# Performance work log

Hardware: AMD Instinct MI355X
Metric: run time of the kernel (lower is better)

Reference implementation:

```python
import jax, jax.numpy as jnp
import numpy as np

IN_DIM = 300   # args.glove_init == 1
MID_DIM = 450  # ceil(1.5 * 300)
BATCH = 131072
NEG_SLOPE = 0.1


def setup_inputs() -> dict:
    key = jax.random.key(0)
    ks = jax.random.split(key, 13)

    def W(k, o, i):
        return jax.random.normal(k, (o, i), jnp.float32) * (1.0 / np.sqrt(i).astype(np.float32))

    def b(k, o):
        return jax.random.normal(k, (o,), jnp.float32) * 0.01

    inp = {"x": jax.random.normal(ks[0], (BATCH, IN_DIM), jnp.float32)}
    # NOT_op: Linear(300->450), LeakyReLU(0.1), Linear(450->300), LeakyReLU(0.1)
    inp["not_W1"] = W(ks[1], MID_DIM, IN_DIM);      inp["not_b1"] = b(ks[2], MID_DIM)
    inp["not_W2"] = W(ks[3], IN_DIM, MID_DIM);      inp["not_b2"] = b(ks[4], IN_DIM)
    # AND_op: Linear(600->450), LeakyReLU, Linear(450->300), LeakyReLU
    inp["and_W1"] = W(ks[5], MID_DIM, 2 * IN_DIM);  inp["and_b1"] = b(ks[6], MID_DIM)
    inp["and_W2"] = W(ks[7], IN_DIM, MID_DIM);      inp["and_b2"] = b(ks[8], IN_DIM)
    # OR_op: same shapes as AND_op
    inp["or_W1"] = W(ks[9], MID_DIM, 2 * IN_DIM);   inp["or_b1"] = b(ks[10], MID_DIM)
    inp["or_W2"] = W(ks[11], IN_DIM, MID_DIM);      inp["or_b2"] = b(ks[12], IN_DIM)
    inp["epoch"] = 1  # epoch <= el_epochs -> el_forward path
    return inp


def _mlp(x, W1, b1, W2, b2):
    # torch Linear: y = x @ W.T + b; LeakyReLU(0.1)
    h = jax.nn.leaky_relu(x @ W1.T + b1, NEG_SLOPE)
    return jax.nn.leaky_relu(h @ W2.T + b2, NEG_SLOPE)


def reference(x, not_W1, not_b1, not_W2, not_b2,
              and_W1, and_b1, and_W2, and_b2,
              or_W1, or_b1, or_W2, or_b2, epoch):
    # el_forward, fully batched (original loops over samples):
    # pairs: (x, NOT(NOT(x))), (x, AND([x,x])), (x, OR([x,x])); MSE over all pairs.
    s2a = _mlp(_mlp(x, not_W1, not_b1, not_W2, not_b2), not_W1, not_b1, not_W2, not_b2)
    xx = jnp.concatenate([x, x], axis=-1)  # [B, 600]
    s2b = _mlp(xx, and_W1, and_b1, and_W2, and_b2)
    s2c = _mlp(xx, or_W1, or_b1, or_W2, or_b2)
    # mean over the stacked 3B pairs == mean of the three per-pair MSEs
    loss = (jnp.mean((x - s2a) ** 2)
            + jnp.mean((x - s2b) ** 2)
            + jnp.mean((x - s2c) ** 2)) / 3.0
    return loss
```

## Files before the change

### kernel.cpp

```cpp
#include <hip/hip_runtime.h>

typedef __attribute__((ext_vector_type(8))) short short8;
typedef __attribute__((ext_vector_type(4))) float f32x4;

#define BATCH   131072
#define IND     300
#define MIDD    450
#define XS      328
#define HS      488
#define BM      64
#define NTHR    512

constexpr int SZ1 = 464 * XS;
constexpr int SZ2 = 304 * HS;
constexpr int O_NOT1 = 0;
constexpr int O_NOT2 = SZ1;
constexpr int O_AND1 = SZ1 + SZ2;
constexpr int O_AND2 = 2 * SZ1 + SZ2;
constexpr int O_OR1  = 2 * SZ1 + 2 * SZ2;
constexpr int O_OR2  = 3 * SZ1 + 2 * SZ2;
constexpr int WS_ELEMS = 3 * SZ1 + 3 * SZ2;

constexpr int XBYTES = BM * XS * 2;
constexpr int HBYTES = BM * HS * 2;
constexpr int LDS_BYTES = XBYTES + HBYTES;

__device__ __forceinline__ unsigned short f2b(float f) {
  unsigned u = __builtin_bit_cast(unsigned, f);
  u = (u + 0x7FFFu + ((u >> 16) & 1u)) >> 16;
  return (unsigned short)u;
}
__device__ __forceinline__ float b2f(unsigned short h) {
  unsigned u = ((unsigned)h) << 16;
  return __builtin_bit_cast(float, u);
}
__device__ __forceinline__ f32x4 mfma16(short8 a, short8 b, f32x4 c) {
  asm("v_mfma_f32_16x16x32_bf16 %0, %1, %2, %0" : "+v"(c) : "v"(a), "v"(b));
  return c;
}

__global__ void prep_weights(const float* __restrict__ nw1, const float* __restrict__ nw2,
                             const float* __restrict__ aw1, const float* __restrict__ aw2,
                             const float* __restrict__ ow1, const float* __restrict__ ow2,
                             unsigned short* __restrict__ ws)
{
  int idx = blockIdx.x * 256 + threadIdx.x;
  if (idx < 3 * SZ1) {
    int r = idx / SZ1, off = idx % SZ1;
    int n = off / XS, k = off % XS;
    float v = 0.f;
    if (n < MIDD && k < IND) {
      if (r == 0) v = nw1[n * IND + k];
      else {
        const float* s = (r == 1) ? aw1 : ow1;
        v = s[n * 2 * IND + k] + s[n * 2 * IND + IND + k];
      }
    }
    int base = (r == 0) ? O_NOT1 : (r == 1) ? O_AND1 : O_OR1;
    ws[base + off] = f2b(v);
  } else if (idx < WS_ELEMS) {
    int i2 = idx - 3 * SZ1;
    int r = i2 / SZ2, off = i2 % SZ2;
    int n = off / HS, k = off % HS;
    float v = 0.f;
    if (n < IND && k < MIDD) {
      const float* s = (r == 0) ? nw2 : (r == 1) ? aw2 : ow2;
      v = s[n * MIDD + k];
    }
    int base = (r == 0) ? O_NOT2 : (r == 1) ? O_AND2 : O_OR2;
    ws[base + off] = f2b(v);
  }
}

template <int KB, int NT, int N, bool MSE>
__device__ __forceinline__ void stage(const unsigned short* __restrict__ IN, int in_stride,
                                      const unsigned short* __restrict__ Wg, int wg_stride,
                                      const float* __restrict__ bias,
                                      unsigned short* __restrict__ Hout,
                                      const unsigned short* __restrict__ XT,
                                      float& sq, int tid, int wn, int l16, int lhi)
{
  constexpr int NJ = (NT + 7) / 8;
  f32x4 acc[4][NJ];
#pragma unroll
  for (int m = 0; m < 4; m++)
#pragma unroll
    for (int j = 0; j < NJ; j++) acc[m][j] = f32x4{0.f, 0.f, 0.f, 0.f};

  const unsigned short* ap[4];
#pragma unroll
  for (int m = 0; m < 4; m++) ap[m] = IN + (m * 16 + l16) * in_stride + lhi * 8;
  const unsigned short* bp[NJ];
#pragma unroll
  for (int j = 0; j < NJ; j++) {
    int nt = wn + 8 * j;
    int row = (nt < NT ? nt : 0) * 16 + l16;
    bp[j] = Wg + row * wg_stride + lhi * 8;
  }

  short8 a0[4], a1[4], b0[NJ], b1[NJ], b2[NJ];

#define LA_(buf, kk)                                                     \
  { _Pragma("unroll") for (int m = 0; m < 4; m++)                        \
      buf[m] = *(const short8*)(ap[m] + (kk) * 32); }
#define LB_(buf, kk)                                                     \
  { _Pragma("unroll") for (int j = 0; j < NJ; j++)                       \
      if (wn + 8 * j < NT) buf[j] = *(const short8*)(bp[j] + (kk) * 32); }

  LB_(b0, 0);
  if (KB > 1) LB_(b1, 1);
  LA_(a0, 0);

#pragma unroll
  for (int kb = 0; kb < KB; kb++) {
    short8* ac = (kb & 1) ? a1 : a0;
    short8* an = (kb & 1) ? a0 : a1;
    short8* bc = (kb % 3 == 0) ? b0 : (kb % 3 == 1) ? b1 : b2;
    short8* bn = ((kb + 2) % 3 == 0) ? b0 : ((kb + 2) % 3 == 1) ? b1 : b2;
    if (kb + 2 < KB) LB_(bn, kb + 2);
    if (kb + 1 < KB) LA_(an, kb + 1);
#pragma unroll
    for (int j = 0; j < NJ; j++) {
      if (wn + 8 * j < NT) {
#pragma unroll
        for (int m = 0; m < 4; m++) acc[m][j] = mfma16(ac[m], bc[j], acc[m][j]);
      }
    }
  }
#undef LA_
#undef LB_

  if (!MSE) __syncthreads();

#pragma unroll
  for (int j = 0; j < NJ; j++) {
    int nt = wn + 8 * j;
    if (nt >= NT) continue;
    int col = nt * 16 + l16;
    bool valid = col < N;
    float bv = valid ? bias[col] : 0.f;
#pragma unroll
    for (int m = 0; m < 4; m++) {
#pragma unroll
      for (int r = 0; r < 4; r++) {
        int row = m * 16 + lhi * 4 + r;
        float v = acc[m][j][r] + bv;
        v = v > 0.f ? v : 0.1f * v;
        if (MSE) {
          if (valid) { float d = b2f(XT[row * XS + col]) - v; sq += d * d; }
        } else {
          if (valid) Hout[row * HS + col] = f2b(v);
        }
      }
    }
  }
  if (!MSE && N == IND) {
    for (int i = tid; i < BM * 20; i += NTHR) {
      int r = i / 20, c = i - r * 20;
      Hout[r * HS + IND + c] = 0;
    }
  }
}

__global__ __launch_bounds__(NTHR, 2)
void fused(const float* __restrict__ x, const unsigned short* __restrict__ ws,
           const float* __restrict__ nb1, const float* __restrict__ nb2,
           const float* __restrict__ ab1, const float* __restrict__ ab2,
           const float* __restrict__ ob1, const float* __restrict__ ob2,
           float* __restrict__ out)
{
  extern __shared__ __align__(16) char smem[];
  unsigned short* X = (unsigned short*)smem;
  unsigned short* H = (unsigned short*)(smem + XBYTES);
  int tid = threadIdx.x, wid = tid >> 6, lane = tid & 63;
  int l16 = lane & 15, lhi = lane >> 4;

  for (int i = tid; i < LDS_BYTES / 4; i += NTHR) ((unsigned*)smem)[i] = 0u;
  __syncthreads();

  int row0 = blockIdx.x * BM;
  for (int i = tid; i < BM * IND; i += NTHR) {
    int r = i / IND, c = i - r * IND;
    X[r * XS + c] = f2b(x[(row0 + r) * IND + c]);
  }
  __syncthreads();

  float sq = 0.f;
  stage<10, 29, MIDD, false>(X, XS, ws + O_NOT1, XS, nb1, H, X, sq, tid, wid, l16, lhi);
  __syncthreads();
  stage<15, 19, IND,  false>(H, HS, ws + O_NOT2, HS, nb2, H, X, sq, tid, wid, l16, lhi);
  __syncthreads();
  stage<10, 29, MIDD, false>(H, HS, ws + O_NOT1, XS, nb1, H, X, sq, tid, wid, l16, lhi);
  __syncthreads();
  stage<15, 19, IND,  true >(H, HS, ws + O_NOT2, HS, nb2, H, X, sq, tid, wid, l16, lhi);
  __syncthreads();
  stage<10, 29, MIDD, false>(X, XS, ws + O_AND1, XS, ab1, H, X, sq, tid, wid, l16, lhi);
  __syncthreads();
  stage<15, 19, IND,  true >(H, HS, ws + O_AND2, HS, ab2, H, X, sq, tid, wid, l16, lhi);
  __syncthreads();
  stage<10, 29, MIDD, false>(X, XS, ws + O_OR1,  XS, ob1, H, X, sq, tid, wid, l16, lhi);
  __syncthreads();
  stage<15, 19, IND,  true >(H, HS, ws + O_OR2,  HS, ob2, H, X, sq, tid, wid, l16, lhi);

#pragma unroll
  for (int off = 32; off > 0; off >>= 1) sq += __shfl_down(sq, off);
  __shared__ float wsum[8];
  if (lane == 0) wsum[wid] = sq;
  __syncthreads();
  if (tid == 0) {
    float s = 0.f;
#pragma unroll
    for (int w = 0; w < 8; w++) s += wsum[w];
    atomicAdd(out, s);
  }
}

__global__ void finalize(float* out) {
  out[0] *= (1.0f / (3.0f * (float)BATCH * (float)IND));
}

extern "C" void kernel_launch(void* const* d_in, const int* in_sizes, int n_in,
                              void* d_out, int out_size, void* d_ws, size_t ws_size,
                              hipStream_t stream) {
  const float* x   = (const float*)d_in[0];
  const float* nw1 = (const float*)d_in[1];
  const float* nb1 = (const float*)d_in[2];
  const float* nw2 = (const float*)d_in[3];
  const float* nb2 = (const float*)d_in[4];
  const float* aw1 = (const float*)d_in[5];
  const float* ab1 = (const float*)d_in[6];
  const float* aw2 = (const float*)d_in[7];
  const float* ab2 = (const float*)d_in[8];
  const float* ow1 = (const float*)d_in[9];
  const float* ob1 = (const float*)d_in[10];
  const float* ow2 = (const float*)d_in[11];
  const float* ob2 = (const float*)d_in[12];
  unsigned short* ws = (unsigned short*)d_ws;
  float* out = (float*)d_out;

  hipMemsetAsync(d_out, 0, sizeof(float), stream);

  int prep_blocks = (WS_ELEMS + 255) / 256;
  prep_weights<<<prep_blocks, 256, 0, stream>>>(nw1, nw2, aw1, aw2, ow1, ow2, ws);

  hipFuncSetAttribute((const void*)fused,
                      hipFuncAttributeMaxDynamicSharedMemorySize, LDS_BYTES);
  fused<<<BATCH / BM, NTHR, LDS_BYTES, stream>>>(x, ws, nb1, nb2, ab1, ab2, ob1, ob2, out);

  finalize<<<1, 1, 0, stream>>>(out);
}
```

Before: 620.8 us.

## Shrink row tile to 48 and raise occupancy to four blocks per CU

Reduces the per-block row tile from 64 to 48 and trims the weight prefetch from triple to double buffering. Together these lower register and LDS use so launch bounds can ask for four 512-thread blocks per CU instead of two. A tail-row guard is added because 131072 is not a multiple of 48. The goal is more waves resident to hide LDS and global load latency, at the cost of less reuse of each weight fragment per MFMA and a shallower prefetch pipeline.

```diff
diff --git a/kernel.cpp b/kernel.cpp
--- a/kernel.cpp
+++ b/kernel.cpp
@@ -8,8 +8,9 @@
 #define MIDD    450
 #define XS      328
 #define HS      488
-#define BM      64
+#define BM      48
 #define NTHR    512
+#define NBLK    ((BATCH + BM - 1) / BM)
 
 constexpr int SZ1 = 464 * XS;
 constexpr int SZ2 = 304 * HS;
@@ -78,18 +79,18 @@
                                       const float* __restrict__ bias,
                                       unsigned short* __restrict__ Hout,
                                       const unsigned short* __restrict__ XT,
-                                      float& sq, int tid, int wn, int l16, int lhi)
+                                      float& sq, int rows, int tid, int wn, int l16, int lhi)
 {
   constexpr int NJ = (NT + 7) / 8;
-  f32x4 acc[4][NJ];
-#pragma unroll
-  for (int m = 0; m < 4; m++)
+  f32x4 acc[3][NJ];
+#pragma unroll
+  for (int m = 0; m < 3; m++)
 #pragma unroll
     for (int j = 0; j < NJ; j++) acc[m][j] = f32x4{0.f, 0.f, 0.f, 0.f};
 
-  const unsigned short* ap[4];
-#pragma unroll
-  for (int m = 0; m < 4; m++) ap[m] = IN + (m * 16 + l16) * in_stride + lhi * 8;
+  const unsigned short* ap[3];
+#pragma unroll
+  for (int m = 0; m < 3; m++) ap[m] = IN + (m * 16 + l16) * in_stride + lhi * 8;
   const unsigned short* bp[NJ];
 #pragma unroll
   for (int j = 0; j < NJ; j++) {
@@ -98,32 +99,31 @@
     bp[j] = Wg + row * wg_stride + lhi * 8;
   }
 
-  short8 a0[4], a1[4], b0[NJ], b1[NJ], b2[NJ];
+  short8 a0[3], a1[3], b0[NJ], b1[NJ];
 
 #define LA_(buf, kk)                                                     \
-  { _Pragma("unroll") for (int m = 0; m < 4; m++)                        \
+  { _Pragma("unroll") for (int m = 0; m < 3; m++)                        \
       buf[m] = *(const short8*)(ap[m] + (kk) * 32); }
 #define LB_(buf, kk)                                                     \
   { _Pragma("unroll") for (int j = 0; j < NJ; j++)                       \
       if (wn + 8 * j < NT) buf[j] = *(const short8*)(bp[j] + (kk) * 32); }
 
   LB_(b0, 0);
-  if (KB > 1) LB_(b1, 1);
   LA_(a0, 0);
 
 #pragma unroll
   for (int kb = 0; kb < KB; kb++) {
     short8* ac = (kb & 1) ? a1 : a0;
     short8* an = (kb & 1) ? a0 : a1;
-    short8* bc = (kb % 3 == 0) ? b0 : (kb % 3 == 1) ? b1 : b2;
-    short8* bn = ((kb + 2) % 3 == 0) ? b0 : ((kb + 2) % 3 == 1) ? b1 : b2;
-    if (kb + 2 < KB) LB_(bn, kb + 2);
+    short8* bc = (kb & 1) ? b1 : b0;
+    short8* bn = (kb & 1) ? b0 : b1;
+    if (kb + 1 < KB) LB_(bn, kb + 1);
     if (kb + 1 < KB) LA_(an, kb + 1);
 #pragma unroll
     for (int j = 0; j < NJ; j++) {
       if (wn + 8 * j < NT) {
 #pragma unroll
-        for (int m = 0; m < 4; m++) acc[m][j] = mfma16(ac[m], bc[j], acc[m][j]);
+        for (int m = 0; m < 3; m++) acc[m][j] = mfma16(ac[m], bc[j], acc[m][j]);
       }
     }
   }
@@ -140,14 +140,14 @@
     bool valid = col < N;
     float bv = valid ? bias[col] : 0.f;
 #pragma unroll
-    for (int m = 0; m < 4; m++) {
+    for (int m = 0; m < 3; m++) {
 #pragma unroll
       for (int r = 0; r < 4; r++) {
         int row = m * 16 + lhi * 4 + r;
         float v = acc[m][j][r] + bv;
         v = v > 0.f ? v : 0.1f * v;
         if (MSE) {
-          if (valid) { float d = b2f(XT[row * XS + col]) - v; sq += d * d; }
+          if (valid && row < rows) { float d = b2f(XT[row * XS + col]) - v; sq += d * d; }
         } else {
           if (valid) Hout[row * HS + col] = f2b(v);
         }
@@ -162,7 +162,7 @@
   }
 }
 
-__global__ __launch_bounds__(NTHR, 2)
+__global__ __launch_bounds__(NTHR, 4)
 void fused(const float* __restrict__ x, const unsigned short* __restrict__ ws,
            const float* __restrict__ nb1, const float* __restrict__ nb2,
            const float* __restrict__ ab1, const float* __restrict__ ab2,
@@ -172,6 +172,7 @@
   extern __shared__ __align__(16) char smem[];
   unsigned short* X = (unsigned short*)smem;
   unsigned short* H = (unsigned short*)(smem + XBYTES);
+  __shared__ float wsum[8];
   int tid = threadIdx.x, wid = tid >> 6, lane = tid & 63;
   int l16 = lane & 15, lhi = lane >> 4;
 
@@ -179,32 +180,32 @@
   __syncthreads();
 
   int row0 = blockIdx.x * BM;
-  for (int i = tid; i < BM * IND; i += NTHR) {
+  int rows = (row0 + BM <= BATCH) ? BM : (BATCH - row0);
+  for (int i = tid; i < rows * IND; i += NTHR) {
     int r = i / IND, c = i - r * IND;
-    X[r * XS + c] = f2b(x[(row0 + r) * IND + c]);
+    X[r * XS + c] = f2b(x[(size_t)(row0 + r) * IND + c]);
   }
   __syncthreads();
 
   float sq = 0.f;
-  stage<10, 29, MIDD, false>(X, XS, ws + O_NOT1, XS, nb1, H, X, sq, tid, wid, l16, lhi);
-  __syncthreads();
-  stage<15, 19, IND,  false>(H, HS, ws + O_NOT2, HS, nb2, H, X, sq, tid, wid, l16, lhi);
-  __syncthreads();
-  stage<10, 29, MIDD, false>(H, HS, ws + O_NOT1, XS, nb1, H, X, sq, tid, wid, l16, lhi);
-  __syncthreads();
-  stage<15, 19, IND,  true >(H, HS, ws + O_NOT2, HS, nb2, H, X, sq, tid, wid, l16, lhi);
-  __syncthreads();
-  stage<10, 29, MIDD, false>(X, XS, ws + O_AND1, XS, ab1, H, X, sq, tid, wid, l16, lhi);
-  __syncthreads();
-  stage<15, 19, IND,  true >(H, HS, ws + O_AND2, HS, ab2, H, X, sq, tid, wid, l16, lhi);
-  __syncthreads();
-  stage<10, 29, MIDD, false>(X, XS, ws + O_OR1,  XS, ob1, H, X, sq, tid, wid, l16, lhi);
-  __syncthreads();
-  stage<15, 19, IND,  true >(H, HS, ws + O_OR2,  HS, ob2, H, X, sq, tid, wid, l16, lhi);
+  stage<10, 29, MIDD, false>(X, XS, ws + O_NOT1, XS, nb1, H, X, sq, rows, tid, wid, l16, lhi);
+  __syncthreads();
+  stage<15, 19, IND,  false>(H, HS, ws + O_NOT2, HS, nb2, H, X, sq, rows, tid, wid, l16, lhi);
+  __syncthreads();
+  stage<10, 29, MIDD, false>(H, HS, ws + O_NOT1, XS, nb1, H, X, sq, rows, tid, wid, l16, lhi);
+  __syncthreads();
+  stage<15, 19, IND,  true >(H, HS, ws + O_NOT2, HS, nb2, H, X, sq, rows, tid, wid, l16, lhi);
+  __syncthreads();
+  stage<10, 29, MIDD, false>(X, XS, ws + O_AND1, XS, ab1, H, X, sq, rows, tid, wid, l16, lhi);
+  __syncthreads();
+  stage<15, 19, IND,  true >(H, HS, ws + O_AND2, HS, ab2, H, X, sq, rows, tid, wid, l16, lhi);
+  __syncthreads();
+  stage<10, 29, MIDD, false>(X, XS, ws + O_OR1,  XS, ob1, H, X, sq, rows, tid, wid, l16, lhi);
+  __syncthreads();
+  stage<15, 19, IND,  true >(H, HS, ws + O_OR2,  HS, ob2, H, X, sq, rows, tid, wid, l16, lhi);
 
 #pragma unroll
   for (int off = 32; off > 0; off >>= 1) sq += __shfl_down(sq, off);
-  __shared__ float wsum[8];
   if (lane == 0) wsum[wid] = sq;
   __syncthreads();
   if (tid == 0) {
@@ -245,7 +246,7 @@
 
   hipFuncSetAttribute((const void*)fused,
                       hipFuncAttributeMaxDynamicSharedMemorySize, LDS_BYTES);
-  fused<<<BATCH / BM, NTHR, LDS_BYTES, stream>>>(x, ws, nb1, nb2, ab1, ab2, ob1, ob2, out);
+  fused<<<NBLK, NTHR, LDS_BYTES, stream>>>(x, ws, nb1, nb2, ab1, ab2, ob1, ob2, out);
 
   finalize<<<1, 1, 0, stream>>>(out);
 }
```

Result: slower. 777.4 us (+25.2%).

## Deepen operand prefetch pipeline, tighten weight strides, relax launch bounds

Applied to the files above, without the earlier changes.

Global-memory weight loads now run four k-steps ahead (five rotating B buffers) and LDS activation loads two steps ahead (three A buffers), up from two and one, to hide more load latency behind MFMAs. The packed bf16 weight workspace uses narrower row strides (320/480 instead of 328/488), which shrinks its footprint. The occupancy hint of 2 blocks per CU is dropped from launch bounds so the compiler can use more registers for the extra buffers. The cost is higher VGPR pressure, which may lower occupancy or cause spills.

```diff
diff --git a/kernel.cpp b/kernel.cpp
--- a/kernel.cpp
+++ b/kernel.cpp
@@ -8,11 +8,13 @@
 #define MIDD    450
 #define XS      328
 #define HS      488
+#define WXS     320
+#define WHS     480
 #define BM      64
 #define NTHR    512
 
-constexpr int SZ1 = 464 * XS;
-constexpr int SZ2 = 304 * HS;
+constexpr int SZ1 = 464 * WXS;
+constexpr int SZ2 = 304 * WHS;
 constexpr int O_NOT1 = 0;
 constexpr int O_NOT2 = SZ1;
 constexpr int O_AND1 = SZ1 + SZ2;
@@ -47,7 +49,7 @@
   int idx = blockIdx.x * 256 + threadIdx.x;
   if (idx < 3 * SZ1) {
     int r = idx / SZ1, off = idx % SZ1;
-    int n = off / XS, k = off % XS;
+    int n = off / WXS, k = off % WXS;
     float v = 0.f;
     if (n < MIDD && k < IND) {
       if (r == 0) v = nw1[n * IND + k];
@@ -61,7 +63,7 @@
   } else if (idx < WS_ELEMS) {
     int i2 = idx - 3 * SZ1;
     int r = i2 / SZ2, off = i2 % SZ2;
-    int n = off / HS, k = off % HS;
+    int n = off / WHS, k = off % WHS;
     float v = 0.f;
     if (n < IND && k < MIDD) {
       const float* s = (r == 0) ? nw2 : (r == 1) ? aw2 : ow2;
@@ -98,7 +100,8 @@
     bp[j] = Wg + row * wg_stride + lhi * 8;
   }
 
-  short8 a0[4], a1[4], b0[NJ], b1[NJ], b2[NJ];
+  short8 a0[4], a1[4], a2[4];
+  short8 b0[NJ], b1[NJ], b2[NJ], b3[NJ], b4[NJ];
 
 #define LA_(buf, kk)                                                     \
   { _Pragma("unroll") for (int m = 0; m < 4; m++)                        \
@@ -107,18 +110,19 @@
   { _Pragma("unroll") for (int j = 0; j < NJ; j++)                       \
       if (wn + 8 * j < NT) buf[j] = *(const short8*)(bp[j] + (kk) * 32); }
 
-  LB_(b0, 0);
-  if (KB > 1) LB_(b1, 1);
-  LA_(a0, 0);
+  LB_(b0, 0); LB_(b1, 1); LB_(b2, 2); LB_(b3, 3);
+  LA_(a0, 0); LA_(a1, 1);
 
 #pragma unroll
   for (int kb = 0; kb < KB; kb++) {
-    short8* ac = (kb & 1) ? a1 : a0;
-    short8* an = (kb & 1) ? a0 : a1;
-    short8* bc = (kb % 3 == 0) ? b0 : (kb % 3 == 1) ? b1 : b2;
-    short8* bn = ((kb + 2) % 3 == 0) ? b0 : ((kb + 2) % 3 == 1) ? b1 : b2;
-    if (kb + 2 < KB) LB_(bn, kb + 2);
-    if (kb + 1 < KB) LA_(an, kb + 1);
+    short8* ac = (kb % 3 == 0) ? a0 : (kb % 3 == 1) ? a1 : a2;
+    short8* an = ((kb + 2) % 3 == 0) ? a0 : ((kb + 2) % 3 == 1) ? a1 : a2;
+    short8* bc = (kb % 5 == 0) ? b0 : (kb % 5 == 1) ? b1 : (kb % 5 == 2) ? b2
+               : (kb % 5 == 3) ? b3 : b4;
+    short8* bn = ((kb + 4) % 5 == 0) ? b0 : ((kb + 4) % 5 == 1) ? b1
+               : ((kb + 4) % 5 == 2) ? b2 : ((kb + 4) % 5 == 3) ? b3 : b4;
+    if (kb + 4 < KB) LB_(bn, kb + 4);
+    if (kb + 2 < KB) LA_(an, kb + 2);
 #pragma unroll
     for (int j = 0; j < NJ; j++) {
       if (wn + 8 * j < NT) {
@@ -162,7 +166,7 @@
   }
 }
 
-__global__ __launch_bounds__(NTHR, 2)
+__global__ __launch_bounds__(NTHR)
 void fused(const float* __restrict__ x, const unsigned short* __restrict__ ws,
            const float* __restrict__ nb1, const float* __restrict__ nb2,
            const float* __restrict__ ab1, const float* __restrict__ ab2,
@@ -172,6 +176,7 @@
   extern __shared__ __align__(16) char smem[];
   unsigned short* X = (unsigned short*)smem;
   unsigned short* H = (unsigned short*)(smem + XBYTES);
+  __shared__ float wsum[8];
   int tid = threadIdx.x, wid = tid >> 6, lane = tid & 63;
   int l16 = lane & 15, lhi = lane >> 4;
 
@@ -181,30 +186,29 @@
   int row0 = blockIdx.x * BM;
   for (int i = tid; i < BM * IND; i += NTHR) {
     int r = i / IND, c = i - r * IND;
-    X[r * XS + c] = f2b(x[(row0 + r) * IND + c]);
+    X[r * XS + c] = f2b(x[(size_t)(row0 + r) * IND + c]);
   }
   __syncthreads();
 
   float sq = 0.f;
-  stage<10, 29, MIDD, false>(X, XS, ws + O_NOT1, XS, nb1, H, X, sq, tid, wid, l16, lhi);
-  __syncthreads();
-  stage<15, 19, IND,  false>(H, HS, ws + O_NOT2, HS, nb2, H, X, sq, tid, wid, l16, lhi);
-  __syncthreads();
-  stage<10, 29, MIDD, false>(H, HS, ws + O_NOT1, XS, nb1, H, X, sq, tid, wid, l16, lhi);
-  __syncthreads();
-  stage<15, 19, IND,  true >(H, HS, ws + O_NOT2, HS, nb2, H, X, sq, tid, wid, l16, lhi);
-  __syncthreads();
-  stage<10, 29, MIDD, false>(X, XS, ws + O_AND1, XS, ab1, H, X, sq, tid, wid, l16, lhi);
-  __syncthreads();
-  stage<15, 19, IND,  true >(H, HS, ws + O_AND2, HS, ab2, H, X, sq, tid, wid, l16, lhi);
-  __syncthreads();
-  stage<10, 29, MIDD, false>(X, XS, ws + O_OR1,  XS, ob1, H, X, sq, tid, wid, l16, lhi);
-  __syncthreads();
-  stage<15, 19, IND,  true >(H, HS, ws + O_OR2,  HS, ob2, H, X, sq, tid, wid, l16, lhi);
+  stage<10, 29, MIDD, false>(X, XS, ws + O_NOT1, WXS, nb1, H, X, sq, tid, wid, l16, lhi);
+  __syncthreads();
+  stage<15, 19, IND,  false>(H, HS, ws + O_NOT2, WHS, nb2, H, X, sq, tid, wid, l16, lhi);
+  __syncthreads();
+  stage<10, 29, MIDD, false>(H, HS, ws + O_NOT1, WXS, nb1, H, X, sq, tid, wid, l16, lhi);
+  __syncthreads();
+  stage<15, 19, IND,  true >(H, HS, ws + O_NOT2, WHS, nb2, H, X, sq, tid, wid, l16, lhi);
+  __syncthreads();
+  stage<10, 29, MIDD, false>(X, XS, ws + O_AND1, WXS, ab1, H, X, sq, tid, wid, l16, lhi);
+  __syncthreads();
+  stage<15, 19, IND,  true >(H, HS, ws + O_AND2, WHS, ab2, H, X, sq, tid, wid, l16, lhi);
+  __syncthreads();
+  stage<10, 29, MIDD, false>(X, XS, ws + O_OR1,  WXS, ob1, H, X, sq, tid, wid, l16, lhi);
+  __syncthreads();
+  stage<15, 19, IND,  true >(H, HS, ws + O_OR2,  WHS, ob2, H, X, sq, tid, wid, l16, lhi);
 
 #pragma unroll
   for (int off = 32; off > 0; off >>= 1) sq += __shfl_down(sq, off);
-  __shared__ float wsum[8];
   if (lane == 0) wsum[wid] = sq;
   __syncthreads();
   if (tid == 0) {
```

Result: no change. 610.3 us (-1.7%).
